# Performance work log

Hardware: AMD Instinct MI355X
Metric: run time of the kernel (lower is better)

Reference implementation:

```python
import jax, jax.numpy as jnp
import numpy as np
from jax import lax

START, STOP = 5, 6
K = 7           # tagset size
NEG = -10000.0  # CRF -inf surrogate used by the original module


def setup_inputs() -> dict:
    key = jax.random.key(0)
    ks = jax.random.split(key, 18)
    B, T, V, E, H = 128, 512, 50000, 300, 50
    G = 4 * H  # stacked LSTM gates (i,f,g,o)
    rn = lambda k, s, sc=0.05: jax.random.normal(k, s, jnp.float32) * sc
    inp = {
        'sentence': jax.random.randint(ks[0], (B, T), 0, V),
        'mask': jnp.ones((B, T), jnp.float32),
        'emb': rn(ks[1], (V, E), 1.0),
        'h0': rn(ks[2], (6, B, H), 1.0),
        'c0': rn(ks[3], (6, B, H), 1.0),
        'w_ih_l0': rn(ks[4], (2, G, E)),
        'w_hh_l0': rn(ks[5], (2, G, H)),
        'b_l0': rn(ks[6], (2, G)),
        'w_ih_l1': rn(ks[7], (2, G, 2 * H)),
        'w_hh_l1': rn(ks[8], (2, G, H)),
        'b_l1': rn(ks[9], (2, G)),
        'w_ih_l2': rn(ks[10], (2, G, 2 * H)),
        'w_hh_l2': rn(ks[11], (2, G, H)),
        'b_l2': rn(ks[12], (2, G)),
        'w_tag': rn(ks[13], (K, 2 * H), 0.1),
        'b_tag': rn(ks[14], (K,), 0.1),
    }
    trans = jax.random.normal(ks[15], (K, K), jnp.float32)
    inp['trans'] = trans.at[START, :].set(NEG).at[:, STOP].set(NEG)
    return inp


def _lstm_dir(x, w_ih, w_hh, b, h0, c0, reverse):
    # x: [B,T,I]; precompute input projections once (big GEMM outside the scan)
    xg = jnp.einsum('bti,gi->btg', x, w_ih) + b  # [B,T,4H]

    def step(carry, xg_t):
        h, c = carry
        g = xg_t + h @ w_hh.T
        i, f, gg, o = jnp.split(g, 4, axis=-1)
        c = jax.nn.sigmoid(f) * c + jax.nn.sigmoid(i) * jnp.tanh(gg)
        h = jax.nn.sigmoid(o) * jnp.tanh(c)
        return (h, c), h

    _, hs = lax.scan(step, (h0, c0), jnp.swapaxes(xg, 0, 1), reverse=reverse)
    return jnp.swapaxes(hs, 0, 1)  # [B,T,H]


def _bilstm_layer(x, w_ih, w_hh, b, h0, c0):
    fwd = _lstm_dir(x, w_ih[0], w_hh[0], b[0], h0[0], c0[0], False)
    bwd = _lstm_dir(x, w_ih[1], w_hh[1], b[1], h0[1], c0[1], True)
    return jnp.concatenate([fwd, bwd], axis=-1)


def reference(sentence, mask, emb, h0, c0,
              w_ih_l0, w_hh_l0, b_l0,
              w_ih_l1, w_hh_l1, b_l1,
              w_ih_l2, w_hh_l2, b_l2,
              w_tag, b_tag, trans):
    # --- BiLSTM feature extractor (mask is all-ones: padded == packed) ---
    x = emb[sentence]  # [B,T,E]
    x = _bilstm_layer(x, w_ih_l0, w_hh_l0, b_l0, h0[0:2], c0[0:2])
    x = _bilstm_layer(x, w_ih_l1, w_hh_l1, b_l1, h0[2:4], c0[2:4])
    x = _bilstm_layer(x, w_ih_l2, w_hh_l2, b_l2, h0[4:6], c0[4:6])
    feats = (x @ w_tag.T + b_tag) * mask[..., None]  # [B,T,K]

    # --- Viterbi decode (matches _viterbi_decode: no STOP transition) ---
    B = feats.shape[0]
    score0 = jnp.full((B, K), NEG, feats.dtype).at[:, START].set(0.0)

    def vstep(score, feat_t):
        m = score[:, None, :] + trans[None, :, :]   # [B, next i, prev j]
        bptr_t = jnp.argmax(m, axis=-1)
        return jnp.max(m, axis=-1) + feat_t, bptr_t

    score, bptr = lax.scan(vstep, score0, jnp.swapaxes(feats, 0, 1))  # bptr [T,B,K]
    best_score = jnp.max(score, axis=-1)
    best_tag = jnp.argmax(score, axis=-1)

    def back(tag, bptr_t):
        prev = jnp.take_along_axis(bptr_t, tag[:, None], axis=1)[:, 0]
        return prev, tag

    _, tags = lax.scan(back, best_tag, bptr, reverse=True)  # [T,B]
    return best_score, jnp.swapaxes(tags, 0, 1)
```

## Files before the change

### kernel.cpp

```cpp
#include <hip/hip_runtime.h>

#define NEGV (-10000.0f)

static constexpr int Bb    = 128;
static constexpr int Tt    = 512;
static constexpr int Mrows = Bb * Tt;
static constexpr int Hh    = 50;
static constexpr int START = 5;

typedef __attribute__((ext_vector_type(8))) short bf16x8;
typedef __attribute__((ext_vector_type(4))) float f32x4;

__device__ __forceinline__ float fsig(float x) {
    return __builtin_amdgcn_rcpf(1.0f + __expf(-x));
}
__device__ __forceinline__ float ftanh(float x) {
    return 2.0f * __builtin_amdgcn_rcpf(1.0f + __expf(-2.0f * x)) - 1.0f;
}
__device__ __forceinline__ unsigned short f2bf(float f) {
    unsigned u = __float_as_uint(f);
    u = (u + 0x7fffu + ((u >> 16) & 1u)) >> 16;
    return (unsigned short)u;
}
#define BF(u) __uint_as_float(((unsigned)(u)) << 16)

__global__ __launch_bounds__(256) void conv_w(
    const float* __restrict__ src, unsigned short* __restrict__ dst,
    int K, int KP)
{
    int gid = blockIdx.x * 256 + threadIdx.x;
    int tot = 448 * KP;
    if (gid >= tot) return;
    int r = gid / KP, c = gid % KP;
    float v = (r < 400 && c < K) ? src[r * K + c] : 0.f;
    dst[gid] = f2bf(v);
}

template <bool GATHER>
__global__ __launch_bounds__(256) void conv_a(
    const float* __restrict__ src, const int* __restrict__ idx,
    unsigned short* __restrict__ dst, int K, int KP, int cpr)
{
    long gid = (long)blockIdx.x * 256 + threadIdx.x;
    long tot = (long)Mrows * cpr;
    if (gid >= tot) return;
    long m = gid / cpr;
    int p = (int)(gid - m * cpr) * 8;
    const float* s = src + (GATHER ? (long)idx[m] : m) * K;
    unsigned u0, u1, u2, u3;
    {
        float x0 = (p + 0 < K) ? s[p + 0] : 0.f;
        float x1 = (p + 1 < K) ? s[p + 1] : 0.f;
        float x2 = (p + 2 < K) ? s[p + 2] : 0.f;
        float x3 = (p + 3 < K) ? s[p + 3] : 0.f;
        float x4 = (p + 4 < K) ? s[p + 4] : 0.f;
        float x5 = (p + 5 < K) ? s[p + 5] : 0.f;
        float x6 = (p + 6 < K) ? s[p + 6] : 0.f;
        float x7 = (p + 7 < K) ? s[p + 7] : 0.f;
        u0 = (unsigned)f2bf(x0) | ((unsigned)f2bf(x1) << 16);
        u1 = (unsigned)f2bf(x2) | ((unsigned)f2bf(x3) << 16);
        u2 = (unsigned)f2bf(x4) | ((unsigned)f2bf(x5) << 16);
        u3 = (unsigned)f2bf(x6) | ((unsigned)f2bf(x7) << 16);
    }
    uint4 v = make_uint4(u0, u1, u2, u3);
    *(uint4*)(dst + m * KP + p) = v;
}

__global__ __launch_bounds__(256) void gemm_mfma(
    const unsigned short* __restrict__ Ab,
    const unsigned short* __restrict__ Wb,
    const float* __restrict__ bias,
    unsigned short* __restrict__ C,
    int KP)
{
    __shared__ unsigned short As[128][40];
    __shared__ unsigned short Ws[64][40];

    const int tid = threadIdx.x;
    const int m0 = blockIdx.x * 128;
    const int n0 = blockIdx.y * 64;

    const int w  = tid >> 6, l = tid & 63;
    const int wm = (w >> 1) * 64;
    const int wn = (w & 1) * 32;
    const int lr = l & 15;
    const int lk = (l >> 4) * 8;

    f32x4 acc[4][2] = {};

    for (int k0 = 0; k0 < KP; k0 += 32) {
        __syncthreads();
        {
            int c = tid;
            int r = c >> 2, p = (c & 3) * 8;
            *(bf16x8*)&As[r][p] = *(const bf16x8*)(Ab + (long)(m0 + r) * KP + k0 + p);
            c = tid + 256;
            r = c >> 2; p = (c & 3) * 8;
            *(bf16x8*)&As[r][p] = *(const bf16x8*)(Ab + (long)(m0 + r) * KP + k0 + p);
            r = tid >> 2; p = (tid & 3) * 8;
            *(bf16x8*)&Ws[r][p] = *(const bf16x8*)(Wb + (long)(n0 + r) * KP + k0 + p);
        }
        __syncthreads();

        bf16x8 af0 = *(const bf16x8*)&As[wm +  0 + lr][lk];
        bf16x8 af1 = *(const bf16x8*)&As[wm + 16 + lr][lk];
        bf16x8 af2 = *(const bf16x8*)&As[wm + 32 + lr][lk];
        bf16x8 af3 = *(const bf16x8*)&As[wm + 48 + lr][lk];
        bf16x8 wf0 = *(const bf16x8*)&Ws[wn +  0 + lr][lk];
        bf16x8 wf1 = *(const bf16x8*)&Ws[wn + 16 + lr][lk];

        acc[0][0] = __builtin_amdgcn_mfma_f32_16x16x32_bf16(af0, wf0, acc[0][0], 0, 0, 0);
        acc[0][1] = __builtin_amdgcn_mfma_f32_16x16x32_bf16(af0, wf1, acc[0][1], 0, 0, 0);
        acc[1][0] = __builtin_amdgcn_mfma_f32_16x16x32_bf16(af1, wf0, acc[1][0], 0, 0, 0);
        acc[1][1] = __builtin_amdgcn_mfma_f32_16x16x32_bf16(af1, wf1, acc[1][1], 0, 0, 0);
        acc[2][0] = __builtin_amdgcn_mfma_f32_16x16x32_bf16(af2, wf0, acc[2][0], 0, 0, 0);
        acc[2][1] = __builtin_amdgcn_mfma_f32_16x16x32_bf16(af2, wf1, acc[2][1], 0, 0, 0);
        acc[3][0] = __builtin_amdgcn_mfma_f32_16x16x32_bf16(af3, wf0, acc[3][0], 0, 0, 0);
        acc[3][1] = __builtin_amdgcn_mfma_f32_16x16x32_bf16(af3, wf1, acc[3][1], 0, 0, 0);
    }

    const int orow = (l >> 4) * 4;
    const int ocol = l & 15;
    #pragma unroll
    for (int a = 0; a < 4; ++a) {
        #pragma unroll
        for (int bb = 0; bb < 2; ++bb) {
            const int col = n0 + wn + bb * 16 + ocol;
            if (col < 400) {
                const float bv = bias[col];
                #pragma unroll
                for (int i = 0; i < 4; ++i) {
                    const long row = m0 + wm + a * 16 + orow + i;
                    C[row * 400 + col] = f2bf(acc[a][bb][i] + bv);
                }
            }
        }
    }
}

#define H(J) __uint_as_float((unsigned)__builtin_amdgcn_readlane((int)__float_as_uint(hreg), (J)))

__global__ void
__attribute__((amdgpu_flat_work_group_size(256, 256), amdgpu_waves_per_eu(1, 1)))
lstm_scan(
    const unsigned short* __restrict__ xg,
    const float* __restrict__ w_hh,
    const float* __restrict__ h0,
    const float* __restrict__ c0,
    float* __restrict__ xout)
{
    const int b    = blockIdx.x & 127;
    const int dir  = blockIdx.x >> 7;
    const int tid  = threadIdx.x;
    const int lane = tid & 63;
    const int wv   = tid >> 6;

    __shared__ float pre[2][200];

    const int gr = (tid < 200) ? tid : 199;

    const float* wr = w_hh + ((long)dir * 200 + gr) * 50;
    float w0  = wr[0],  w1  = wr[1],  w2  = wr[2],  w3  = wr[3],  w4  = wr[4];
    float w5  = wr[5],  w6  = wr[6],  w7  = wr[7],  w8  = wr[8],  w9  = wr[9];
    float w10 = wr[10], w11 = wr[11], w12 = wr[12], w13 = wr[13], w14 = wr[14];
    float w15 = wr[15], w16 = wr[16], w17 = wr[17], w18 = wr[18], w19 = wr[19];
    float w20 = wr[20], w21 = wr[21], w22 = wr[22], w23 = wr[23], w24 = wr[24];
    float w25 = wr[25], w26 = wr[26], w27 = wr[27], w28 = wr[28], w29 = wr[29];
    float w30 = wr[30], w31 = wr[31], w32 = wr[32], w33 = wr[33], w34 = wr[34];
    float w35 = wr[35], w36 = wr[36], w37 = wr[37], w38 = wr[38], w39 = wr[39];
    float w40 = wr[40], w41 = wr[41], w42 = wr[42], w43 = wr[43], w44 = wr[44];
    float w45 = wr[45], w46 = wr[46], w47 = wr[47], w48 = wr[48], w49 = wr[49];
    asm volatile("" : "+v"(w0), "+v"(w1), "+v"(w2), "+v"(w3), "+v"(w4),
                      "+v"(w5), "+v"(w6), "+v"(w7), "+v"(w8), "+v"(w9));
    asm volatile("" : "+v"(w10), "+v"(w11), "+v"(w12), "+v"(w13), "+v"(w14),
                      "+v"(w15), "+v"(w16), "+v"(w17), "+v"(w18), "+v"(w19));
    asm volatile("" : "+v"(w20), "+v"(w21), "+v"(w22), "+v"(w23), "+v"(w24),
                      "+v"(w25), "+v"(w26), "+v"(w27), "+v"(w28), "+v"(w29));
    asm volatile("" : "+v"(w30), "+v"(w31), "+v"(w32), "+v"(w33), "+v"(w34),
                      "+v"(w35), "+v"(w36), "+v"(w37), "+v"(w38), "+v"(w39));
    asm volatile("" : "+v"(w40), "+v"(w41), "+v"(w42), "+v"(w43), "+v"(w44),
                      "+v"(w45), "+v"(w46), "+v"(w47), "+v"(w48), "+v"(w49));

    float hreg = 0.f, c = 0.f;
    if (lane < 50) {
        c    = c0[((long)dir * Bb + b) * Hh + lane];
        hreg = h0[((long)dir * Bb + b) * Hh + lane];
    }
    __syncthreads();

    const long rowbase = (long)b * Tt;
    const unsigned short* xbase = xg + rowbase * 400 + dir * 200 + gr;
    float* op = xout + rowbase * 100 + dir * 50 + lane;

    #define XLD(s)  xbase[(long)(dir ? (Tt - 1 - (s)) : (s)) * 400]
    #define TTOF(s) (dir ? (Tt - 1 - (s)) : (s))

    #define STEP(PRE, XIN, TT) do {                                         \
        if (tid < 200) {                                                    \
            float s0 = BF(XIN), s1 = 0.f, s2 = 0.f, s3 = 0.f;               \
            s0 += w0 *H(0);  s1 += w1 *H(1);  s2 += w2 *H(2);  s3 += w3 *H(3);  \
            s0 += w4 *H(4);  s1 += w5 *H(5);  s2 += w6 *H(6);  s3 += w7 *H(7);  \
            s0 += w8 *H(8);  s1 += w9 *H(9);  s2 += w10*H(10); s3 += w11*H(11); \
            s0 += w12*H(12); s1 += w13*H(13); s2 += w14*H(14); s3 += w15*H(15); \
            s0 += w16*H(16); s1 += w17*H(17); s2 += w18*H(18); s3 += w19*H(19); \
            s0 += w20*H(20); s1 += w21*H(21); s2 += w22*H(22); s3 += w23*H(23); \
            s0 += w24*H(24); s1 += w25*H(25); s2 += w26*H(26); s3 += w27*H(27); \
            s0 += w28*H(28); s1 += w29*H(29); s2 += w30*H(30); s3 += w31*H(31); \
            s0 += w32*H(32); s1 += w33*H(33); s2 += w34*H(34); s3 += w35*H(35); \
            s0 += w36*H(36); s1 += w37*H(37); s2 += w38*H(38); s3 += w39*H(39); \
            s0 += w40*H(40); s1 += w41*H(41); s2 += w42*H(42); s3 += w43*H(43); \
            s0 += w44*H(44); s1 += w45*H(45); s2 += w46*H(46); s3 += w47*H(47); \
            s0 += w48*H(48); s1 += w49*H(49);                               \
            (PRE)[tid] = (s0 + s1) + (s2 + s3);                             \
        }                                                                   \
        asm volatile("s_waitcnt lgkmcnt(0)\n\ts_barrier" ::: "memory");     \
        if (lane < 50) {                                                    \
            const float gi = fsig((PRE)[lane]);                             \
            const float gf = fsig((PRE)[50 + lane]);                        \
            const float gc = ftanh((PRE)[100 + lane]);                      \
            const float go = fsig((PRE)[150 + lane]);                       \
            c = gf * c + gi * gc;                                           \
            hreg = go * ftanh(c);                                           \
            if (wv == 0) op[(long)(TT) * 100] = hreg;                       \
        }                                                                   \
    } while (0)

    unsigned xc0 = XLD(0), xc1 = XLD(1), xc2 = XLD(2), xc3 = XLD(3);
    unsigned xn0 = 0, xn1 = 0, xn2 = 0, xn3 = 0;

    for (int blk = 0; blk < Tt / 4; ++blk) {
        const int s0i = blk * 4;
        if (blk < Tt / 4 - 1) {
            xn0 = XLD(s0i + 4); xn1 = XLD(s0i + 5);
            xn2 = XLD(s0i + 6); xn3 = XLD(s0i + 7);
        }
        STEP(pre[0], xc0, TTOF(s0i + 0));
        STEP(pre[1], xc1, TTOF(s0i + 1));
        STEP(pre[0], xc2, TTOF(s0i + 2));
        STEP(pre[1], xc3, TTOF(s0i + 3));
        xc0 = xn0; xc1 = xn1; xc2 = xn2; xc3 = xn3;
    }
    #undef STEP
    #undef XLD
    #undef TTOF
}

__global__ __launch_bounds__(256) void feats_kernel(
    const float* __restrict__ x,
    const float* __restrict__ w_tag,
    const float* __restrict__ b_tag,
    const float* __restrict__ mask,
    float* __restrict__ feats)
{
    const int gid = blockIdx.x * 256 + threadIdx.x;
    const int row = gid >> 3;
    const int i   = gid & 7;
    if (row >= Mrows) return;
    if (i == 7) { feats[(long)row * 8 + 7] = 0.f; return; }
    const float4* xr = (const float4*)(x + (long)row * 100);
    const float4* wr = (const float4*)(w_tag + (long)i * 100);
    float acc = b_tag[i];
    #pragma unroll
    for (int q = 0; q < 25; ++q) {
        float4 a = xr[q];
        float4 b = wr[q];
        acc += a.x * b.x + a.y * b.y + a.z * b.z + a.w * b.w;
    }
    feats[(long)row * 8 + i] = acc * mask[row];
}

__global__ __launch_bounds__(64) void viterbi_fwd(
    const float* __restrict__ feats,
    const float* __restrict__ trans,
    unsigned int* __restrict__ bptrw,
    float* __restrict__ best_score,
    int* __restrict__ best_tag)
{
    const int lane = threadIdx.x;
    const int sub  = lane >> 3;
    const int i    = lane & 7;
    const int b    = blockIdx.x * 8 + sub;
    const int base = lane & 56;

    float tr[7];
    #pragma unroll
    for (int j = 0; j < 7; ++j) tr[j] = (i < 7) ? trans[i * 7 + j] : -1e30f;

    float score = (i == START) ? 0.0f : NEGV;
    const long fb = (long)b * Tt;

    float featc = feats[(fb + 0) * 8 + i];
    for (int t = 0; t < Tt; ++t) {
        float featn = (t + 1 < Tt) ? feats[(fb + t + 1) * 8 + i] : 0.f;
        float best = -3.4e38f;
        int bp = 0;
        #pragma unroll
        for (int j = 0; j < 7; ++j) {
            float sj = __shfl(score, base | j, 64);
            float m = sj + tr[j];
            if (m > best) { best = m; bp = j; }
        }
        if (i < 7) score = best + featc;
        unsigned v = (i < 7) ? ((unsigned)bp << (3 * i)) : 0u;
        v |= __shfl_xor(v, 1, 64);
        v |= __shfl_xor(v, 2, 64);
        v |= __shfl_xor(v, 4, 64);
        if (i == 0) bptrw[(long)t * Bb + b] = v;
        featc = featn;
    }

    float bestv = score;
    int bt = 0;
    #pragma unroll
    for (int j = 1; j < 7; ++j) {
        float sj = __shfl(score, base | j, 64);
        if (i == 0 && sj > bestv) { bestv = sj; bt = j; }
    }
    if (i == 0) {
        best_score[b] = bestv;
        best_tag[b]   = bt;
    }
}

__global__ __launch_bounds__(128) void backtrack(
    const unsigned int* __restrict__ bptrw,
    const int* __restrict__ best_tag,
    float* __restrict__ out_tags)
{
    const int b = threadIdx.x;
    if (b >= Bb) return;
    const long fb = (long)b * Tt;
    int tag = best_tag[b];
    out_tags[fb + Tt - 1] = (float)tag;
    #pragma unroll 8
    for (int t = Tt - 1; t >= 1; --t) {
        unsigned w = bptrw[(long)t * Bb + b];
        tag = (w >> (3 * tag)) & 7;
        out_tags[fb + t - 1] = (float)tag;
    }
}

extern "C" void kernel_launch(void* const* d_in, const int* in_sizes, int n_in,
                              void* d_out, int out_size, void* d_ws, size_t ws_size,
                              hipStream_t stream)
{
    const int*   sent    = (const int*)  d_in[0];
    const float* mask    = (const float*)d_in[1];
    const float* emb     = (const float*)d_in[2];
    const float* h0      = (const float*)d_in[3];
    const float* c0      = (const float*)d_in[4];
    const float* w_ih_l0 = (const float*)d_in[5];
    const float* w_hh_l0 = (const float*)d_in[6];
    const float* b_l0    = (const float*)d_in[7];
    const float* w_ih_l1 = (const float*)d_in[8];
    const float* w_hh_l1 = (const float*)d_in[9];
    const float* b_l1    = (const float*)d_in[10];
    const float* w_ih_l2 = (const float*)d_in[11];
    const float* w_hh_l2 = (const float*)d_in[12];
    const float* b_l2    = (const float*)d_in[13];
    const float* w_tag   = (const float*)d_in[14];
    const float* b_tag   = (const float*)d_in[15];
    const float* trans   = (const float*)d_in[16];

    float* out = (float*)d_out;
    char* ws = (char*)d_ws;

    unsigned short* xg    = (unsigned short*)(ws);
    float*          xa    = (float*)(ws + 52428800L);
    float*          xb    = (float*)(ws + 78643200L);
    unsigned short* AbR   = (unsigned short*)(ws + 104857600L);
    float*          feats = (float*)(ws + 146800640L);
    unsigned*       bptrw = (unsigned*)(ws + 148897792L);
    unsigned short* Wb0   = (unsigned short*)(ws + 149159936L);
    unsigned short* Wb1   = (unsigned short*)(ws + 149446656L);
    unsigned short* Wb2   = (unsigned short*)(ws + 149561344L);
    int*            btag  = (int*)(ws + 149676032L);

    dim3 gridG(Mrows / 128, 7);

    conv_w<<<(448 * 320 + 255) / 256, 256, 0, stream>>>(w_ih_l0, Wb0, 300, 320);
    conv_w<<<(448 * 128 + 255) / 256, 256, 0, stream>>>(w_ih_l1, Wb1, 100, 128);
    conv_w<<<(448 * 128 + 255) / 256, 256, 0, stream>>>(w_ih_l2, Wb2, 100, 128);

    conv_a<true><<<(Mrows * 40 + 255) / 256, 256, 0, stream>>>(emb, sent, AbR, 300, 320, 40);
    gemm_mfma<<<gridG, 256, 0, stream>>>(AbR, Wb0, b_l0, xg, 320);
    lstm_scan<<<256, 256, 0, stream>>>(xg, w_hh_l0, h0 + 0 * Bb * Hh, c0 + 0 * Bb * Hh, xa);

    conv_a<false><<<(Mrows * 16 + 255) / 256, 256, 0, stream>>>(xa, nullptr, AbR, 100, 128, 16);
    gemm_mfma<<<gridG, 256, 0, stream>>>(AbR, Wb1, b_l1, xg, 128);
    lstm_scan<<<256, 256, 0, stream>>>(xg, w_hh_l1, h0 + 2 * Bb * Hh, c0 + 2 * Bb * Hh, xb);

    conv_a<false><<<(Mrows * 16 + 255) / 256, 256, 0, stream>>>(xb, nullptr, AbR, 100, 128, 16);
    gemm_mfma<<<gridG, 256, 0, stream>>>(AbR, Wb2, b_l2, xg, 128);
    lstm_scan<<<256, 256, 0, stream>>>(xg, w_hh_l2, h0 + 4 * Bb * Hh, c0 + 4 * Bb * Hh, xa);

    feats_kernel<<<Mrows * 8 / 256, 256, 0, stream>>>(xa, w_tag, b_tag, mask, feats);
    viterbi_fwd<<<Bb / 8, 64, 0, stream>>>(feats, trans, bptrw, out, btag);
    backtrack<<<1, 128, 0, stream>>>(bptrw, btag, out + Bb);
}
```

Baseline: 1.192 ms.

## Run LSTM recurrence in a single wave with fp16 dot2 and packed hidden state

The LSTM scan kernel goes from four waves per sequence to one. Each lane now holds the four gate rows for one hidden unit as packed fp16 weights and accumulates with fdot2 over readlane-broadcast packed hidden pairs. This removes the shared-memory gate exchange and the per-step block barrier, and halves the number of broadcast reads. In exchange the recurrent weights and hidden state lose precision to fp16, and each lane does four times the serial dot work.

Measured after the change: 1.247 ms. +4.7%, slower.

```diff
diff --git a/kernel.cpp b/kernel.cpp
--- a/kernel.cpp
+++ b/kernel.cpp
@@ -10,6 +10,7 @@
 
 typedef __attribute__((ext_vector_type(8))) short bf16x8;
 typedef __attribute__((ext_vector_type(4))) float f32x4;
+typedef __attribute__((ext_vector_type(2))) _Float16 h2t;
 
 __device__ __forceinline__ float fsig(float x) {
     return __builtin_amdgcn_rcpf(1.0f + __expf(-x));
@@ -138,10 +139,20 @@
     }
 }
 
-#define H(J) __uint_as_float((unsigned)__builtin_amdgcn_readlane((int)__float_as_uint(hreg), (J)))
+#if __has_builtin(__builtin_amdgcn_fdot2)
+#define DOT2(W, HH, A) A = __builtin_amdgcn_fdot2(W, HH, A, false)
+#else
+#define DOT2(W, HH, A) A += (float)(W).x * (float)(HH).x + (float)(W).y * (float)(HH).y
+#endif
+
+#define LDW(P, Q) __builtin_bit_cast(unsigned, (h2t){(_Float16)(P)[2*(Q)], (_Float16)(P)[2*(Q)+1]})
+#define PKH(A, B) __builtin_bit_cast(h2t, __builtin_amdgcn_cvt_pkrtz((A), (B)))
+#define LA10(x0,x1,x2,x3,x4,x5,x6,x7,x8,x9) \
+    asm volatile("" : "+v"(x0), "+v"(x1), "+v"(x2), "+v"(x3), "+v"(x4), \
+                      "+v"(x5), "+v"(x6), "+v"(x7), "+v"(x8), "+v"(x9))
 
 __global__ void
-__attribute__((amdgpu_flat_work_group_size(256, 256), amdgpu_waves_per_eu(1, 1)))
+__attribute__((amdgpu_flat_work_group_size(64, 64), amdgpu_waves_per_eu(1, 1)))
 lstm_scan(
     const unsigned short* __restrict__ xg,
     const float* __restrict__ w_hh,
@@ -151,98 +162,142 @@
 {
     const int b    = blockIdx.x & 127;
     const int dir  = blockIdx.x >> 7;
-    const int tid  = threadIdx.x;
-    const int lane = tid & 63;
-    const int wv   = tid >> 6;
-
-    __shared__ float pre[2][200];
-
-    const int gr = (tid < 200) ? tid : 199;
-
-    const float* wr = w_hh + ((long)dir * 200 + gr) * 50;
-    float w0  = wr[0],  w1  = wr[1],  w2  = wr[2],  w3  = wr[3],  w4  = wr[4];
-    float w5  = wr[5],  w6  = wr[6],  w7  = wr[7],  w8  = wr[8],  w9  = wr[9];
-    float w10 = wr[10], w11 = wr[11], w12 = wr[12], w13 = wr[13], w14 = wr[14];
-    float w15 = wr[15], w16 = wr[16], w17 = wr[17], w18 = wr[18], w19 = wr[19];
-    float w20 = wr[20], w21 = wr[21], w22 = wr[22], w23 = wr[23], w24 = wr[24];
-    float w25 = wr[25], w26 = wr[26], w27 = wr[27], w28 = wr[28], w29 = wr[29];
-    float w30 = wr[30], w31 = wr[31], w32 = wr[32], w33 = wr[33], w34 = wr[34];
-    float w35 = wr[35], w36 = wr[36], w37 = wr[37], w38 = wr[38], w39 = wr[39];
-    float w40 = wr[40], w41 = wr[41], w42 = wr[42], w43 = wr[43], w44 = wr[44];
-    float w45 = wr[45], w46 = wr[46], w47 = wr[47], w48 = wr[48], w49 = wr[49];
-    asm volatile("" : "+v"(w0), "+v"(w1), "+v"(w2), "+v"(w3), "+v"(w4),
-                      "+v"(w5), "+v"(w6), "+v"(w7), "+v"(w8), "+v"(w9));
-    asm volatile("" : "+v"(w10), "+v"(w11), "+v"(w12), "+v"(w13), "+v"(w14),
-                      "+v"(w15), "+v"(w16), "+v"(w17), "+v"(w18), "+v"(w19));
-    asm volatile("" : "+v"(w20), "+v"(w21), "+v"(w22), "+v"(w23), "+v"(w24),
-                      "+v"(w25), "+v"(w26), "+v"(w27), "+v"(w28), "+v"(w29));
-    asm volatile("" : "+v"(w30), "+v"(w31), "+v"(w32), "+v"(w33), "+v"(w34),
-                      "+v"(w35), "+v"(w36), "+v"(w37), "+v"(w38), "+v"(w39));
-    asm volatile("" : "+v"(w40), "+v"(w41), "+v"(w42), "+v"(w43), "+v"(w44),
-                      "+v"(w45), "+v"(w46), "+v"(w47), "+v"(w48), "+v"(w49));
+    const int lane = threadIdx.x;
+    const int u    = (lane < 50) ? lane : 49;
+
+    const float* r0 = w_hh + (long)dir * 10000 + (long)u * 50;
+    const float* r1 = r0 + 2500;
+    const float* r2 = r0 + 5000;
+    const float* r3 = r0 + 7500;
+
+    unsigned wi0=LDW(r0,0),wi1=LDW(r0,1),wi2=LDW(r0,2),wi3=LDW(r0,3),wi4=LDW(r0,4);
+    unsigned wi5=LDW(r0,5),wi6=LDW(r0,6),wi7=LDW(r0,7),wi8=LDW(r0,8),wi9=LDW(r0,9);
+    unsigned wi10=LDW(r0,10),wi11=LDW(r0,11),wi12=LDW(r0,12),wi13=LDW(r0,13),wi14=LDW(r0,14);
+    unsigned wi15=LDW(r0,15),wi16=LDW(r0,16),wi17=LDW(r0,17),wi18=LDW(r0,18),wi19=LDW(r0,19);
+    unsigned wi20=LDW(r0,20),wi21=LDW(r0,21),wi22=LDW(r0,22),wi23=LDW(r0,23),wi24=LDW(r0,24);
+    unsigned wf0=LDW(r1,0),wf1=LDW(r1,1),wf2=LDW(r1,2),wf3=LDW(r1,3),wf4=LDW(r1,4);
+    unsigned wf5=LDW(r1,5),wf6=LDW(r1,6),wf7=LDW(r1,7),wf8=LDW(r1,8),wf9=LDW(r1,9);
+    unsigned wf10=LDW(r1,10),wf11=LDW(r1,11),wf12=LDW(r1,12),wf13=LDW(r1,13),wf14=LDW(r1,14);
+    unsigned wf15=LDW(r1,15),wf16=LDW(r1,16),wf17=LDW(r1,17),wf18=LDW(r1,18),wf19=LDW(r1,19);
+    unsigned wf20=LDW(r1,20),wf21=LDW(r1,21),wf22=LDW(r1,22),wf23=LDW(r1,23),wf24=LDW(r1,24);
+    unsigned wg0=LDW(r2,0),wg1=LDW(r2,1),wg2=LDW(r2,2),wg3=LDW(r2,3),wg4=LDW(r2,4);
+    unsigned wg5=LDW(r2,5),wg6=LDW(r2,6),wg7=LDW(r2,7),wg8=LDW(r2,8),wg9=LDW(r2,9);
+    unsigned wg10=LDW(r2,10),wg11=LDW(r2,11),wg12=LDW(r2,12),wg13=LDW(r2,13),wg14=LDW(r2,14);
+    unsigned wg15=LDW(r2,15),wg16=LDW(r2,16),wg17=LDW(r2,17),wg18=LDW(r2,18),wg19=LDW(r2,19);
+    unsigned wg20=LDW(r2,20),wg21=LDW(r2,21),wg22=LDW(r2,22),wg23=LDW(r2,23),wg24=LDW(r2,24);
+    unsigned wo0=LDW(r3,0),wo1=LDW(r3,1),wo2=LDW(r3,2),wo3=LDW(r3,3),wo4=LDW(r3,4);
+    unsigned wo5=LDW(r3,5),wo6=LDW(r3,6),wo7=LDW(r3,7),wo8=LDW(r3,8),wo9=LDW(r3,9);
+    unsigned wo10=LDW(r3,10),wo11=LDW(r3,11),wo12=LDW(r3,12),wo13=LDW(r3,13),wo14=LDW(r3,14);
+    unsigned wo15=LDW(r3,15),wo16=LDW(r3,16),wo17=LDW(r3,17),wo18=LDW(r3,18),wo19=LDW(r3,19);
+    unsigned wo20=LDW(r3,20),wo21=LDW(r3,21),wo22=LDW(r3,22),wo23=LDW(r3,23),wo24=LDW(r3,24);
+
+    LA10(wi0,wi1,wi2,wi3,wi4,wi5,wi6,wi7,wi8,wi9);
+    LA10(wi10,wi11,wi12,wi13,wi14,wi15,wi16,wi17,wi18,wi19);
+    LA10(wi20,wi21,wi22,wi23,wi24,wf0,wf1,wf2,wf3,wf4);
+    LA10(wf5,wf6,wf7,wf8,wf9,wf10,wf11,wf12,wf13,wf14);
+    LA10(wf15,wf16,wf17,wf18,wf19,wf20,wf21,wf22,wf23,wf24);
+    LA10(wg0,wg1,wg2,wg3,wg4,wg5,wg6,wg7,wg8,wg9);
+    LA10(wg10,wg11,wg12,wg13,wg14,wg15,wg16,wg17,wg18,wg19);
+    LA10(wg20,wg21,wg22,wg23,wg24,wo0,wo1,wo2,wo3,wo4);
+    LA10(wo5,wo6,wo7,wo8,wo9,wo10,wo11,wo12,wo13,wo14);
+    LA10(wo15,wo16,wo17,wo18,wo19,wo20,wo21,wo22,wo23,wo24);
 
     float hreg = 0.f, c = 0.f;
     if (lane < 50) {
         c    = c0[((long)dir * Bb + b) * Hh + lane];
         hreg = h0[((long)dir * Bb + b) * Hh + lane];
     }
-    __syncthreads();
+
+    const int upk  = (lane < 25) ? lane : 24;
+    const int idxA = (2 * upk) << 2;
+    const int idxB = idxA + 4;
+    #define BPERM(IDX) __uint_as_float((unsigned)__builtin_amdgcn_ds_bpermute((IDX), (int)__float_as_uint(hreg)))
+    h2t hpk = PKH(BPERM(idxA), BPERM(idxB));
 
     const long rowbase = (long)b * Tt;
-    const unsigned short* xbase = xg + rowbase * 400 + dir * 200 + gr;
+    const unsigned short* xbase = xg + rowbase * 400 + dir * 200 + u;
     float* op = xout + rowbase * 100 + dir * 50 + lane;
 
-    #define XLD(s)  xbase[(long)(dir ? (Tt - 1 - (s)) : (s)) * 400]
     #define TTOF(s) (dir ? (Tt - 1 - (s)) : (s))
 
-    #define STEP(PRE, XIN, TT) do {                                         \
-        if (tid < 200) {                                                    \
-            float s0 = BF(XIN), s1 = 0.f, s2 = 0.f, s3 = 0.f;               \
-            s0 += w0 *H(0);  s1 += w1 *H(1);  s2 += w2 *H(2);  s3 += w3 *H(3);  \
-            s0 += w4 *H(4);  s1 += w5 *H(5);  s2 += w6 *H(6);  s3 += w7 *H(7);  \
-            s0 += w8 *H(8);  s1 += w9 *H(9);  s2 += w10*H(10); s3 += w11*H(11); \
-            s0 += w12*H(12); s1 += w13*H(13); s2 += w14*H(14); s3 += w15*H(15); \
-            s0 += w16*H(16); s1 += w17*H(17); s2 += w18*H(18); s3 += w19*H(19); \
-            s0 += w20*H(20); s1 += w21*H(21); s2 += w22*H(22); s3 += w23*H(23); \
-            s0 += w24*H(24); s1 += w25*H(25); s2 += w26*H(26); s3 += w27*H(27); \
-            s0 += w28*H(28); s1 += w29*H(29); s2 += w30*H(30); s3 += w31*H(31); \
-            s0 += w32*H(32); s1 += w33*H(33); s2 += w34*H(34); s3 += w35*H(35); \
-            s0 += w36*H(36); s1 += w37*H(37); s2 += w38*H(38); s3 += w39*H(39); \
-            s0 += w40*H(40); s1 += w41*H(41); s2 += w42*H(42); s3 += w43*H(43); \
-            s0 += w44*H(44); s1 += w45*H(45); s2 += w46*H(46); s3 += w47*H(47); \
-            s0 += w48*H(48); s1 += w49*H(49);                               \
-            (PRE)[tid] = (s0 + s1) + (s2 + s3);                             \
-        }                                                                   \
-        asm volatile("s_waitcnt lgkmcnt(0)\n\ts_barrier" ::: "memory");     \
-        if (lane < 50) {                                                    \
-            const float gi = fsig((PRE)[lane]);                             \
-            const float gf = fsig((PRE)[50 + lane]);                        \
-            const float gc = ftanh((PRE)[100 + lane]);                      \
-            const float go = fsig((PRE)[150 + lane]);                       \
-            c = gf * c + gi * gc;                                           \
-            hreg = go * ftanh(c);                                           \
-            if (wv == 0) op[(long)(TT) * 100] = hreg;                       \
-        }                                                                   \
+    #define DD(K, WI, WF, WG, WO, AI, AF, AG, AO) { \
+        h2t hh = __builtin_bit_cast(h2t, (unsigned)__builtin_amdgcn_readlane(hpki, K)); \
+        DOT2(__builtin_bit_cast(h2t, WI), hh, AI); \
+        DOT2(__builtin_bit_cast(h2t, WF), hh, AF); \
+        DOT2(__builtin_bit_cast(h2t, WG), hh, AG); \
+        DOT2(__builtin_bit_cast(h2t, WO), hh, AO); }
+
+    #define STEP(QI, QF, QG, QO, TT) do { \
+        float ai0 = BF(QI), ai1 = 0.f, af0 = BF(QF), af1 = 0.f; \
+        float ag0 = BF(QG), ag1 = 0.f, ao0 = BF(QO), ao1 = 0.f; \
+        const int hpki = (int)__builtin_bit_cast(unsigned, hpk); \
+        DD(0,  wi0, wf0, wg0, wo0,  ai0,af0,ag0,ao0) \
+        DD(1,  wi1, wf1, wg1, wo1,  ai1,af1,ag1,ao1) \
+        DD(2,  wi2, wf2, wg2, wo2,  ai0,af0,ag0,ao0) \
+        DD(3,  wi3, wf3, wg3, wo3,  ai1,af1,ag1,ao1) \
+        DD(4,  wi4, wf4, wg4, wo4,  ai0,af0,ag0,ao0) \
+        DD(5,  wi5, wf5, wg5, wo5,  ai1,af1,ag1,ao1) \
+        DD(6,  wi6, wf6, wg6, wo6,  ai0,af0,ag0,ao0) \
+        DD(7,  wi7, wf7, wg7, wo7,  ai1,af1,ag1,ao1) \
+        DD(8,  wi8, wf8, wg8, wo8,  ai0,af0,ag0,ao0) \
+        DD(9,  wi9, wf9, wg9, wo9,  ai1,af1,ag1,ao1) \
+        DD(10, wi10,wf10,wg10,wo10, ai0,af0,ag0,ao0) \
+        DD(11, wi11,wf11,wg11,wo11, ai1,af1,ag1,ao1) \
+        DD(12, wi12,wf12,wg12,wo12, ai0,af0,ag0,ao0) \
+        DD(13, wi13,wf13,wg13,wo13, ai1,af1,ag1,ao1) \
+        DD(14, wi14,wf14,wg14,wo14, ai0,af0,ag0,ao0) \
+        DD(15, wi15,wf15,wg15,wo15, ai1,af1,ag1,ao1) \
+        DD(16, wi16,wf16,wg16,wo16, ai0,af0,ag0,ao0) \
+        DD(17, wi17,wf17,wg17,wo17, ai1,af1,ag1,ao1) \
+        DD(18, wi18,wf18,wg18,wo18, ai0,af0,ag0,ao0) \
+        DD(19, wi19,wf19,wg19,wo19, ai1,af1,ag1,ao1) \
+        DD(20, wi20,wf20,wg20,wo20, ai0,af0,ag0,ao0) \
+        DD(21, wi21,wf21,wg21,wo21, ai1,af1,ag1,ao1) \
+        DD(22, wi22,wf22,wg22,wo22, ai0,af0,ag0,ao0) \
+        DD(23, wi23,wf23,wg23,wo23, ai1,af1,ag1,ao1) \
+        DD(24, wi24,wf24,wg24,wo24, ai0,af0,ag0,ao0) \
+        const float gi = fsig(ai0 + ai1); \
+        const float gf = fsig(af0 + af1); \
+        const float gc = ftanh(ag0 + ag1); \
+        const float go = fsig(ao0 + ao1); \
+        c = gf * c + gi * gc; \
+        hreg = go * ftanh(c); \
+        if (lane < 50) op[(long)(TT) * 100] = hreg; \
+        hpk = PKH(BPERM(idxA), BPERM(idxB)); \
     } while (0)
 
-    unsigned xc0 = XLD(0), xc1 = XLD(1), xc2 = XLD(2), xc3 = XLD(3);
-    unsigned xn0 = 0, xn1 = 0, xn2 = 0, xn3 = 0;
+    unsigned qa0, qb0, qc0, qd0, qa1, qb1, qc1, qd1;
+    unsigned qa2, qb2, qc2, qd2, qa3, qb3, qc3, qd3;
+    unsigned na0, nb0, nc0, nd0, na1, nb1, nc1, nd1;
+    unsigned na2, nb2, nc2, nd2, na3, nb3, nc3, nd3;
+    #define XL4(s, A, B, C, D) { \
+        const unsigned short* p = xbase + (long)TTOF(s) * 400; \
+        A = p[0]; B = p[50]; C = p[100]; D = p[150]; }
+    XL4(0, qa0, qb0, qc0, qd0) XL4(1, qa1, qb1, qc1, qd1)
+    XL4(2, qa2, qb2, qc2, qd2) XL4(3, qa3, qb3, qc3, qd3)
+    na0=nb0=nc0=nd0=na1=nb1=nc1=nd1=0;
+    na2=nb2=nc2=nd2=na3=nb3=nc3=nd3=0;
 
     for (int blk = 0; blk < Tt / 4; ++blk) {
         const int s0i = blk * 4;
         if (blk < Tt / 4 - 1) {
-            xn0 = XLD(s0i + 4); xn1 = XLD(s0i + 5);
-            xn2 = XLD(s0i + 6); xn3 = XLD(s0i + 7);
+            XL4(s0i + 4, na0, nb0, nc0, nd0) XL4(s0i + 5, na1, nb1, nc1, nd1)
+            XL4(s0i + 6, na2, nb2, nc2, nd2) XL4(s0i + 7, na3, nb3, nc3, nd3)
         }
-        STEP(pre[0], xc0, TTOF(s0i + 0));
-        STEP(pre[1], xc1, TTOF(s0i + 1));
-        STEP(pre[0], xc2, TTOF(s0i + 2));
-        STEP(pre[1], xc3, TTOF(s0i + 3));
-        xc0 = xn0; xc1 = xn1; xc2 = xn2; xc3 = xn3;
+        STEP(qa0, qb0, qc0, qd0, TTOF(s0i + 0));
+        STEP(qa1, qb1, qc1, qd1, TTOF(s0i + 1));
+        STEP(qa2, qb2, qc2, qd2, TTOF(s0i + 2));
+        STEP(qa3, qb3, qc3, qd3, TTOF(s0i + 3));
+        qa0=na0; qb0=nb0; qc0=nc0; qd0=nd0;
+        qa1=na1; qb1=nb1; qc1=nc1; qd1=nd1;
+        qa2=na2; qb2=nb2; qc2=nc2; qd2=nd2;
+        qa3=na3; qb3=nb3; qc3=nc3; qd3=nd3;
     }
     #undef STEP
-    #undef XLD
+    #undef DD
+    #undef XL4
     #undef TTOF
+    #undef BPERM
 }
 
 __global__ __launch_bounds__(256) void feats_kernel(
@@ -384,15 +439,15 @@
 
     conv_a<true><<<(Mrows * 40 + 255) / 256, 256, 0, stream>>>(emb, sent, AbR, 300, 320, 40);
     gemm_mfma<<<gridG, 256, 0, stream>>>(AbR, Wb0, b_l0, xg, 320);
-    lstm_scan<<<256, 256, 0, stream>>>(xg, w_hh_l0, h0 + 0 * Bb * Hh, c0 + 0 * Bb * Hh, xa);
+    lstm_scan<<<256, 64, 0, stream>>>(xg, w_hh_l0, h0 + 0 * Bb * Hh, c0 + 0 * Bb * Hh, xa);
 
     conv_a<false><<<(Mrows * 16 + 255) / 256, 256, 0, stream>>>(xa, nullptr, AbR, 100, 128, 16);
     gemm_mfma<<<gridG, 256, 0, stream>>>(AbR, Wb1, b_l1, xg, 128);
-    lstm_scan<<<256, 256, 0, stream>>>(xg, w_hh_l1, h0 + 2 * Bb * Hh, c0 + 2 * Bb * Hh, xb);
+    lstm_scan<<<256, 64, 0, stream>>>(xg, w_hh_l1, h0 + 2 * Bb * Hh, c0 + 2 * Bb * Hh, xb);
 
     conv_a<false><<<(Mrows * 16 + 255) / 256, 256, 0, stream>>>(xb, nullptr, AbR, 100, 128, 16);
     gemm_mfma<<<gridG, 256, 0, stream>>>(AbR, Wb2, b_l2, xg, 128);
-    lstm_scan<<<256, 256, 0, stream>>>(xg, w_hh_l2, h0 + 4 * Bb * Hh, c0 + 4 * Bb * Hh, xa);
+    lstm_scan<<<256, 64, 0, stream>>>(xg, w_hh_l2, h0 + 4 * Bb * Hh, c0 + 4 * Bb * Hh, xa);
 
     feats_kernel<<<Mrows * 8 / 256, 256, 0, stream>>>(xa, w_tag, b_tag, mask, feats);
     viterbi_fwd<<<Bb / 8, 64, 0, stream>>>(feats, trans, bptrw, out, btag);
```
